# Kernel tuning notes

Measured on AMD Instinct MI355X. Metric: run time of the kernel, lower is better.

## Reference

```python
import jax, jax.numpy as jnp
import numpy as np
import math

B, C, IMG, E, H, L, FF, D, NCLS = 4, 3, 64, 256, 8, 512, 4, 4, 1000
N = IMG * IMG  # 4096 pixel tokens
HS = H * E    # head_size = embedding_size * heads (per original code)


def setup_inputs() -> dict:
    key = jax.random.key(0)
    ks = jax.random.split(key, 32)
    s = 0.02
    nrm = lambda k, shape: (jax.random.normal(k, shape, jnp.float32) * s)
    inp = {
        "x": jax.random.normal(ks[0], (B, C, N), jnp.float32),
        "conv_w": nrm(ks[1], (E, C)),                 # 1x1 conv1d kernel
        "conv_b": jnp.zeros((E,), jnp.float32),
        "pos_emb": nrm(ks[2], (N, E)),
        "latents": jax.random.normal(ks[3], (L, E), jnp.float32),
        # cross-attention (queries from latents, keys/values from image tokens)
        "ca_wq": nrm(ks[4], (E, HS)),
        "ca_wk": nrm(ks[5], (E, HS)),
        "ca_wv": nrm(ks[6], (E, HS)),
        "ca_wu": nrm(ks[7], (HS, E)),
        "ca_bu": jnp.zeros((E,), jnp.float32),
        "ca_ln_g": jnp.ones((E,), jnp.float32),
        "ca_ln_b": jnp.zeros((E,), jnp.float32),
        # transformer blocks, stacked along depth for lax.scan
        "blk_wq": nrm(ks[8], (D, E, HS)),
        "blk_wk": nrm(ks[9], (D, E, HS)),
        "blk_wv": nrm(ks[10], (D, E, HS)),
        "blk_wu": nrm(ks[11], (D, HS, E)),
        "blk_bu": jnp.zeros((D, E), jnp.float32),
        "blk_ln1_g": jnp.ones((D, E), jnp.float32),
        "blk_ln1_b": jnp.zeros((D, E), jnp.float32),
        "blk_w1": nrm(ks[12], (D, E, FF * E)),
        "blk_b1": jnp.zeros((D, FF * E), jnp.float32),
        "blk_w2": nrm(ks[13], (D, FF * E, E)),
        "blk_b2": jnp.zeros((D, E), jnp.float32),
        "blk_ln2_g": jnp.ones((D, E), jnp.float32),
        "blk_ln2_b": jnp.zeros((D, E), jnp.float32),
        "cls_w": nrm(ks[14], (E, NCLS)),
        "cls_b": jnp.zeros((NCLS,), jnp.float32),
        "heads": H,
    }
    return inp


def _ln(x, g, b):
    m = jnp.mean(x, axis=-1, keepdims=True)
    v = jnp.mean(jnp.square(x - m), axis=-1, keepdims=True)
    return g * (x - m) * jax.lax.rsqrt(v + 1e-5) + b


def _mha(q_in, kv_in, wq, wk, wv, wu, bu, heads):
    # Faithful to original: each head has dim = embedding_size (head_size = heads*emb),
    # and the scale is sqrt(emb // heads).
    b, nq, e = q_in.shape
    nk = kv_in.shape[1]
    q = (q_in @ wq).reshape(b, nq, heads, e)
    k = (kv_in @ wk).reshape(b, nk, heads, e)
    v = (kv_in @ wv).reshape(b, nk, heads, e)
    scale = 1.0 / math.sqrt(e // heads)
    w = jax.nn.softmax(jnp.einsum('bqhe,bkhe->bhqk', q, k) * scale, axis=-1)
    a = jnp.einsum('bhqk,bkhe->bqhe', w, v).reshape(b, nq, heads * e)
    return a @ wu + bu


def reference(x, conv_w, conv_b, pos_emb, latents,
              ca_wq, ca_wk, ca_wv, ca_wu, ca_bu, ca_ln_g, ca_ln_b,
              blk_wq, blk_wk, blk_wv, blk_wu, blk_bu,
              blk_ln1_g, blk_ln1_b, blk_w1, blk_b1, blk_w2, blk_b2,
              blk_ln2_g, blk_ln2_b, cls_w, cls_b, heads):
    bsz = x.shape[0]
    # 1x1 conv1d over flattened pixels: (B, C, N) -> (B, N, E), plus positions
    tokens = jnp.einsum('bcn,ec->bne', x, conv_w) + conv_b + pos_emb
    # latents as queries, image tokens as keys/values (cross-attention)
    z = jnp.broadcast_to(latents, (bsz,) + latents.shape)
    z = _ln(_mha(z, tokens, ca_wq, ca_wk, ca_wv, ca_wu, ca_bu, heads) + z,
            ca_ln_g, ca_ln_b)
    # dropout is identity in eval mode

    def block(z, p):
        wq, wk, wv, wu, bu, g1, b1, w1, c1, w2, c2, g2, b2 = p
        z = _ln(_mha(z, z, wq, wk, wv, wu, bu, heads) + z, g1, b1)
        h = jax.nn.gelu(z @ w1 + c1, approximate=False) @ w2 + c2
        z = _ln(h + z, g2, b2)
        return z, None

    z, _ = jax.lax.scan(block, z,
                        (blk_wq, blk_wk, blk_wv, blk_wu, blk_bu,
                         blk_ln1_g, blk_ln1_b, blk_w1, blk_b1,
                         blk_w2, blk_b2, blk_ln2_g, blk_ln2_b))
    # global average over latents, then classifier
    return jnp.mean(z, axis=1) @ cls_w + cls_b
```

## Files before the change

### kernel.cpp

```cpp
#include <hip/hip_runtime.h>
#include <hip/hip_bf16.h>
#include <math.h>


typedef __attribute__((ext_vector_type(8))) short s8v;
typedef __attribute__((ext_vector_type(4))) float f32x4;
typedef __attribute__((ext_vector_type(16))) float f32x16;
typedef __attribute__((ext_vector_type(4))) unsigned u32x4;

__device__ __forceinline__ short f2b(float f) {
  union { float f; unsigned u; } a; a.f = f;
  unsigned r = a.u + 0x7fff + ((a.u >> 16) & 1);
  return (short)(r >> 16);
}
__device__ __forceinline__ float b2f(short s) {
  union { unsigned u; float f; } a; a.u = ((unsigned)(unsigned short)s) << 16;
  return a.f;
}
__device__ __forceinline__ unsigned cvtpk(float lo, float hi) {
  unsigned r;
  asm("v_cvt_pk_bf16_f32 %0, %1, %2" : "=v"(r) : "v"(lo), "v"(hi));
  return r;
}

__device__ __forceinline__ void gl16(const void* gp, void* lp) {
  __builtin_amdgcn_global_load_lds(
      (const __attribute__((address_space(1))) unsigned int*)gp,
      (__attribute__((address_space(3))) unsigned int*)lp, 16, 0, 0);
}

__global__ __launch_bounds__(256) void k_tokens2(
    const float* __restrict__ x, const float* __restrict__ cw,
    const float* __restrict__ cb, const float* __restrict__ pe,
    short* __restrict__ tok, short* __restrict__ tokT)
{
  int b = blockIdx.y, n0 = blockIdx.x * 32;
  int e = threadIdx.x;
  float c0 = cw[e * 3], c1 = cw[e * 3 + 1], c2 = cw[e * 3 + 2], cbv = cb[e];
  const float* xb = x + b * 12288 + n0;
  short acc[32];
#pragma unroll
  for (int i = 0; i < 32; ++i) {
    int n = n0 + i;
    float s = cbv + pe[n * 256 + e] + xb[i] * c0 + xb[4096 + i] * c1 + xb[8192 + i] * c2;
    short v = f2b(s);
    tok[((long)b * 4096 + n) * 256 + e] = v;
    acc[i] = v;
  }
  short* tr = tokT + ((long)b * 256 + e) * 4096 + n0;
#pragma unroll
  for (int i = 0; i < 4; ++i)
    *reinterpret_cast<s8v*>(tr + i * 8) = *reinterpret_cast<s8v*>(acc + i * 8);
}

struct TrJob {
  const float* src; short* dst;
  int R, C; long sIn, sOut;
  int mode, tilesPerZ, z, tileBase;
  float scale;
};
struct TrJobs { TrJob j[11]; };

__global__ __launch_bounds__(256) void k_trbatch(TrJobs jb, int njobs)
{
  __shared__ float t[32][33];
  int tb = blockIdx.x, ji = 0;
#pragma unroll
  for (int k = 1; k < 11; ++k)
    if (k < njobs && tb >= jb.j[k].tileBase) ji = k;
  TrJob J = jb.j[ji];
  int local = tb - J.tileBase;
  if (J.mode == 1) {
    long o = (long)local * 8192 + threadIdx.x;
#pragma unroll
    for (int k = 0; k < 32; ++k)
      J.dst[o + k * 256] = f2b(J.src[o + k * 256] * J.scale);
    return;
  }
  int zi = local / J.tilesPerZ, ti = local - zi * J.tilesPerZ;
  int ntx = J.C >> 5;
  int tx = ti % ntx, ty = ti / ntx;
  const float* ib = J.src + (long)zi * J.sIn;
  short* ob = J.dst + (long)zi * J.sOut;
  int c0 = tx * 32, r0 = ty * 32;
  int lx = threadIdx.x & 31, ly = threadIdx.x >> 5;
#pragma unroll
  for (int i = 0; i < 4; ++i)
    t[ly * 4 + i][lx] = ib[(long)(r0 + ly * 4 + i) * J.C + c0 + lx];
  __syncthreads();
#pragma unroll
  for (int i = 0; i < 4; ++i)
    ob[(long)(c0 + ly * 4 + i) * J.R + r0 + lx] = f2b(t[lx][ly * 4 + i] * J.scale);
}

template<int EPI>
__global__ __launch_bounds__(256) void k_mgemm(
    const short* __restrict__ A, const short* __restrict__ Bt,
    void* __restrict__ Cv, const float* __restrict__ bias,
    int K, int lda, int ldb, int ldc,
    long sA, long sB, long sC, int zdA, int zmA, int zdB, int zmB)
{
  __shared__ char As[8192];
  __shared__ char Bs[8192];
  int z = blockIdx.z;
  const short* Ab = A + ((long)((z / zdA) % zmA)) * sA;
  const short* Bb = Bt + ((long)((z / zdB) % zmB)) * sB;
  int t = threadIdx.x;
  int lane = t & 63, w = t >> 6;
  int wr = w >> 1, wc = w & 1;
  int g = lane >> 4, l15 = lane & 15;
  long row0 = (long)blockIdx.y * 128, col0 = (long)blockIdx.x * 128;
  const f32x4 zz = {0.f, 0.f, 0.f, 0.f};
  f32x4 acc[4][4];
#pragma unroll
  for (int m = 0; m < 4; ++m)
#pragma unroll
    for (int n = 0; n < 4; ++n) acc[m][n] = zz;

  auto mload = [&](s8v* aa, s8v* bb, int kk) {
#pragma unroll
    for (int i = 0; i < 2; ++i) {
      int r = i * 64 + (t >> 2), c = t & 3;
      aa[i] = *(const s8v*)&Ab[(row0 + r) * (long)lda + kk + c * 8];
      bb[i] = *(const s8v*)&Bb[(col0 + r) * (long)ldb + kk + c * 8];
    }
  };
  auto mstore = [&](s8v* aa, s8v* bb) {
#pragma unroll
    for (int i = 0; i < 2; ++i) {
      int r = i * 64 + (t >> 2), c = t & 3;
      int off = (r * 64 + c * 16) ^ ((r & 7) << 4);
      *(s8v*)&As[off] = aa[i];
      *(s8v*)&Bs[off] = bb[i];
    }
  };
  auto mcomp = [&]() {
    s8v af[4], bfr[4];
#pragma unroll
    for (int m = 0; m < 4; ++m) {
      int r = wr * 64 + m * 16 + l15;
      af[m] = *(const s8v*)&As[(r * 64 + g * 16) ^ ((r & 7) << 4)];
    }
#pragma unroll
    for (int n = 0; n < 4; ++n) {
      int r = wc * 64 + n * 16 + l15;
      bfr[n] = *(const s8v*)&Bs[(r * 64 + g * 16) ^ ((r & 7) << 4)];
    }
#pragma unroll
    for (int m = 0; m < 4; ++m)
#pragma unroll
      for (int n = 0; n < 4; ++n)
        acc[m][n] = __builtin_amdgcn_mfma_f32_16x16x32_bf16(af[m], bfr[n], acc[m][n], 0, 0, 0);
  };

  s8v a0[2], b0[2], a1[2], b1[2];
  mload(a0, b0, 0);
  for (int k0 = 0; k0 < K; k0 += 64) {
    __syncthreads(); mstore(a0, b0); __syncthreads();
    mload(a1, b1, k0 + 32);
    mcomp();
    __syncthreads(); mstore(a1, b1); __syncthreads();
    if (k0 + 64 < K) mload(a0, b0, k0 + 64);
    mcomp();
  }

  long zo = (long)z * sC;
#pragma unroll
  for (int m = 0; m < 4; ++m)
#pragma unroll
    for (int n = 0; n < 4; ++n)
#pragma unroll
      for (int r = 0; r < 4; ++r) {
        long rr = row0 + wr * 64 + m * 16 + g * 4 + r;
        long cc = col0 + wc * 64 + n * 16 + l15;
        float v = acc[m][n][r];
        if (EPI == 1) {
          v += bias[cc];
          v = 0.5f * v * (1.f + erff(v * 0.70710678118654752f));
        }
        if (EPI == 2)
          ((float*)Cv)[zo + rr * ldc + cc] = v;
        else
          ((short*)Cv)[zo + rr * ldc + cc] = f2b(v);
      }
}

__global__ __launch_bounds__(512, 2) void k_mflash8(
    const short* __restrict__ Qp, const short* __restrict__ Kp,
    const short* __restrict__ Vtp, short* __restrict__ Opart,
    float* __restrict__ MLp,
    int nk, int ldq, int ldk, int ldvt,
    long qh, long qb, long kh, long kb, long vh, long vb)
{
  __shared__ char pool[131072];
  int t = threadIdx.x, lane = t & 63, w = t >> 6;
  int l31 = lane & 31, hi = lane >> 5;
  int h = blockIdx.y, b = blockIdx.z;
  int kv = blockIdx.x & 3, qblk = blockIdx.x >> 2;
  const short* Q  = Qp  + (long)h * qh + (long)b * qb;
  const short* Kg = Kp  + (long)h * kh + (long)b * kb;
  const short* Vg = Vtp + (long)h * vh + (long)b * vb;
  int q0w = qblk * 256 + w * 32;
  int nkq = nk >> 2;
  int NIT = nkq >> 6;
  long k0 = (long)kv * nkq;

  s8v qf[16];
  {
    const short* Qrow = Q + (long)(q0w + l31) * ldq + hi * 8;
#pragma unroll
    for (int s = 0; s < 16; ++s) qf[s] = *(const s8v*)(Qrow + s * 16);
  }

  const char* KgB = (const char*)Kg;
  const char* VgB = (const char*)Vg;
  unsigned koff[4], voff[4];
#pragma unroll
  for (int c = 0; c < 4; ++c) {
    int r = 8 * w + 2 * c + hi;
    koff[c] = (unsigned)((k0 + r) * (long)ldk * 2) + ((l31 ^ (r & 31)) << 4);
    int rv = 32 * w + 8 * c + (lane >> 3);
    voff[c] = (unsigned)(((long)rv * ldvt + k0) * 2) + (((lane & 7) ^ (lane >> 3)) << 4);
  }
  const unsigned kStep = (unsigned)(64 * ldk * 2);

  auto stage = [&](int bsel) {
    char* kd = pool + bsel * 65536 + (w << 12);
    char* vd = kd + 32768;
#pragma unroll
    for (int c = 0; c < 4; ++c) { gl16(KgB + koff[c], kd + c * 1024); koff[c] += kStep; }
#pragma unroll
    for (int c = 0; c < 4; ++c) { gl16(VgB + voff[c], vd + c * 1024); voff[c] += 128; }
  };

  f32x16 accO[8];
#pragma unroll
  for (int n = 0; n < 8; ++n)
#pragma unroll
    for (int i = 0; i < 16; ++i) accO[n][i] = 0.f;
  float mrow = -1e30f, lrow = 0.f;

  stage(0);

  for (int it = 0; it < NIT; ++it) {
    int cur = it & 1;
    asm volatile("s_waitcnt vmcnt(0)" ::: "memory");
    __syncthreads();
    if (it + 1 < NIT) stage(cur ^ 1);
    const char* kls = pool + cur * 65536;
    const char* vls = kls + 32768;

    f32x16 sacc[2];
#pragma unroll
    for (int i = 0; i < 16; ++i) { sacc[0][i] = 0.f; sacc[1][i] = 0.f; }
    __builtin_amdgcn_s_setprio(1);
#pragma unroll
    for (int tt = 0; tt < 2; ++tt) {
      int r = tt * 32 + l31;
#pragma unroll
      for (int s = 0; s < 16; ++s) {
        s8v kf = *(const s8v*)&kls[r * 512 + (((2 * s + hi) ^ l31) << 4)];
        sacc[tt] = __builtin_amdgcn_mfma_f32_32x32x16_bf16(kf, qf[s], sacc[tt], 0, 0, 0);
      }
    }
    __builtin_amdgcn_s_setprio(0);

    float mt = sacc[0][0];
#pragma unroll
    for (int i = 1; i < 16; ++i) mt = fmaxf(mt, sacc[0][i]);
#pragma unroll
    for (int i = 0; i < 16; ++i) mt = fmaxf(mt, sacc[1][i]);
    mt = fmaxf(mt, __shfl_xor(mt, 32));
    if (__any(mt - mrow > 8.f)) {
      float mn = fmaxf(mrow, mt);
      float al = __expf(mrow - mn);
      mrow = mn; lrow *= al;
#pragma unroll
      for (int r = 0; r < 16; ++r) {
        float alr = __shfl(al, (r & 3) + 8 * (r >> 2) + 4 * hi);
#pragma unroll
        for (int n = 0; n < 8; ++n) accO[n][r] *= alr;
      }
    }
    float ls = 0.f;
#pragma unroll
    for (int tt = 0; tt < 2; ++tt)
#pragma unroll
      for (int i = 0; i < 16; ++i) {
        float p = __expf(sacc[tt][i] - mrow);
        sacc[tt][i] = p; ls += p;
      }
    ls += __shfl_xor(ls, 32);
    lrow += ls;

    s8v pa[4];
#pragma unroll
    for (int s = 0; s < 4; ++s) {
      int tt = s >> 1, r0 = (s & 1) * 8;
      unsigned w0 = cvtpk(sacc[tt][r0 + 0], sacc[tt][r0 + 1]);
      unsigned w1 = cvtpk(sacc[tt][r0 + 2], sacc[tt][r0 + 3]);
      unsigned w2 = cvtpk(sacc[tt][r0 + 4], sacc[tt][r0 + 5]);
      unsigned w3 = cvtpk(sacc[tt][r0 + 6], sacc[tt][r0 + 7]);
      unsigned x0 = (unsigned)__shfl_xor((int)w0, 32);
      unsigned x1 = (unsigned)__shfl_xor((int)w1, 32);
      unsigned x2 = (unsigned)__shfl_xor((int)w2, 32);
      unsigned x3 = (unsigned)__shfl_xor((int)w3, 32);
      u32x4 pw;
      pw.x = hi ? x2 : w0;
      pw.y = hi ? x3 : w1;
      pw.z = hi ? w2 : x0;
      pw.w = hi ? w3 : x1;
      pa[s] = *(s8v*)&pw;
    }

    __builtin_amdgcn_s_setprio(1);
#pragma unroll
    for (int n = 0; n < 8; ++n) {
      int rv = n * 32 + l31;
#pragma unroll
      for (int s2 = 0; s2 < 4; ++s2) {
        s8v vf = *(const s8v*)&vls[rv * 128 + (((2 * s2 + hi) ^ (l31 & 7)) << 4)];
        accO[n] = __builtin_amdgcn_mfma_f32_32x32x16_bf16(pa[s2], vf, accO[n], 0, 0, 0);
      }
    }
    __builtin_amdgcn_s_setprio(0);
  }

  long prow = (((long)kv * 4 + b) * 8 + h) * 512;
  short* Ob = Opart + prow * 256;
  float* MLb = MLp + prow * 2;
  if (lane < 32) {
    MLb[(q0w + l31) * 2] = mrow;
    MLb[(q0w + l31) * 2 + 1] = lrow;
  }
  char* freebuf = pool + ((((NIT - 1) & 1) ^ 1) << 16);
  float* st = (float*)(freebuf + w * 4096);
  int orow = lane >> 1, ohalf = lane & 1;
#pragma unroll
  for (int n = 0; n < 8; ++n) {
#pragma unroll
    for (int r = 0; r < 16; ++r) {
      int ql = (r & 3) + 8 * (r >> 2) + 4 * hi;
      st[ql * 32 + l31] = accO[n][r];
    }
    short obuf[16];
#pragma unroll
    for (int jj = 0; jj < 4; ++jj) {
      f32x4 v = *(const f32x4*)&st[orow * 32 + ohalf * 16 + jj * 4];
      obuf[jj * 4 + 0] = f2b(v.x); obuf[jj * 4 + 1] = f2b(v.y);
      obuf[jj * 4 + 2] = f2b(v.z); obuf[jj * 4 + 3] = f2b(v.w);
    }
    short* dst = Ob + (long)(q0w + orow) * 256 + n * 32 + ohalf * 16;
    *(s8v*)(dst) = *(s8v*)&obuf[0];
    *(s8v*)(dst + 8) = *(s8v*)&obuf[8];
  }
}

__global__ __launch_bounds__(512) void k_fcomb(
    const short* __restrict__ Op, const float* __restrict__ ML,
    short* __restrict__ O)
{
  int d = threadIdx.x & 255;
  int q = blockIdx.x * 2 + (threadIdx.x >> 8);
  int h = blockIdx.y, b = blockIdx.z;
  const long kvs = 4L * 8 * 512;
  long r0 = ((long)b * 8 + h) * 512 + q;
  float mm[4], ll[4], m = -1e30f;
#pragma unroll
  for (int kv = 0; kv < 4; ++kv) {
    mm[kv] = ML[(kv * kvs + r0) * 2];
    ll[kv] = ML[(kv * kvs + r0) * 2 + 1];
    m = fmaxf(m, mm[kv]);
  }
  float wv[4], lsum = 0.f;
#pragma unroll
  for (int kv = 0; kv < 4; ++kv) { wv[kv] = __expf(mm[kv] - m); lsum += ll[kv] * wv[kv]; }
  float inv = 1.f / lsum, acc = 0.f;
#pragma unroll
  for (int kv = 0; kv < 4; ++kv)
    acc += b2f(Op[(kv * kvs + r0) * 256 + d]) * wv[kv];
  O[(long)b * 1048576 + (long)q * 2048 + h * 256 + d] = f2b(acc * inv);
}

__global__ __launch_bounds__(256) void k_bias_res_ln(
    const float* __restrict__ Yp, int nPart, long pStride,
    const float* __restrict__ bias,
    const float* __restrict__ res, int resMod,
    const float* __restrict__ g, const float* __restrict__ bta,
    float* __restrict__ out, short* __restrict__ out_bf)
{
  __shared__ float red[4];
  int row = blockIdx.x, e = threadIdx.x;
  float v = bias[e] + res[(long)(row % resMod) * 256 + e];
  for (int s = 0; s < nPart; ++s) v += Yp[s * pStride + (long)row * 256 + e];
  float s1 = v;
#pragma unroll
  for (int o = 32; o > 0; o >>= 1) s1 += __shfl_down(s1, o);
  if ((e & 63) == 0) red[e >> 6] = s1;
  __syncthreads();
  float mean = (red[0] + red[1] + red[2] + red[3]) * (1.f / 256.f);
  float d = v - mean;
  __syncthreads();
  float s2 = d * d;
#pragma unroll
  for (int o = 32; o > 0; o >>= 1) s2 += __shfl_down(s2, o);
  if ((e & 63) == 0) red[e >> 6] = s2;
  __syncthreads();
  float var = (red[0] + red[1] + red[2] + red[3]) * (1.f / 256.f);
  float o = g[e] * d * rsqrtf(var + 1e-5f) + bta[e];
  out[(long)row * 256 + e] = o;
  out_bf[(long)row * 256 + e] = f2b(o);
}

__global__ __launch_bounds__(256) void k_meancls(
    const float* __restrict__ z, const float* __restrict__ w,
    const float* __restrict__ bias, float* __restrict__ out)
{
  __shared__ float zms[256];
  int b = blockIdx.y, e = threadIdx.x;
  float s = 0.f;
  for (int l = 0; l < 512; ++l) s += z[((long)b * 512 + l) * 256 + e];
  zms[e] = s * (1.f / 512.f);
  __syncthreads();
  int j = blockIdx.x * 256 + e;
  if (j >= 1000) return;
  float acc = bias[j];
  for (int e2 = 0; e2 < 256; ++e2) acc += zms[e2] * w[e2 * 1000 + j];
  out[b * 1000 + j] = acc;
}

extern "C" void kernel_launch(void* const* d_in, const int* in_sizes, int n_in,
                              void* d_out, int out_size, void* d_ws, size_t ws_size,
                              hipStream_t stream)
{
  (void)in_sizes; (void)n_in; (void)out_size; (void)ws_size;
  const float* x       = (const float*)d_in[0];
  const float* conv_w  = (const float*)d_in[1];
  const float* conv_b  = (const float*)d_in[2];
  const float* pos_emb = (const float*)d_in[3];
  const float* latents = (const float*)d_in[4];
  const float* ca_wq   = (const float*)d_in[5];
  const float* ca_wk   = (const float*)d_in[6];
  const float* ca_wv   = (const float*)d_in[7];
  const float* ca_wu   = (const float*)d_in[8];
  const float* ca_bu   = (const float*)d_in[9];
  const float* ca_ln_g = (const float*)d_in[10];
  const float* ca_ln_b = (const float*)d_in[11];
  const float* blk_wq  = (const float*)d_in[12];
  const float* blk_wk  = (const float*)d_in[13];
  const float* blk_wv  = (const float*)d_in[14];
  const float* blk_wu  = (const float*)d_in[15];
  const float* blk_bu  = (const float*)d_in[16];
  const float* blk_ln1_g = (const float*)d_in[17];
  const float* blk_ln1_b = (const float*)d_in[18];
  const float* blk_w1  = (const float*)d_in[19];
  const float* blk_b1  = (const float*)d_in[20];
  const float* blk_w2  = (const float*)d_in[21];
  const float* blk_b2  = (const float*)d_in[22];
  const float* blk_ln2_g = (const float*)d_in[23];
  const float* blk_ln2_b = (const float*)d_in[24];
  const float* cls_w   = (const float*)d_in[25];
  const float* cls_b   = (const float*)d_in[26];
  float* out = (float*)d_out;

  short* wqT_ca = (short*)d_ws;
  short* wkT_ca = wqT_ca + 524288;
  short* wuT_ca = wkT_ca + 524288;
  short* wv_ca  = wuT_ca + 524288;
  short* lat_bf = wv_ca + 524288;
  short* wqkT   = lat_bf + 131072;
  short* wvT    = wqkT + 4194304;
  short* wuT_b  = wvT + 2097152;
  short* w1T    = wuT_b + 2097152;
  short* w2T    = w1T + 1048576;
  short* tok_bf = w2T + 1048576;
  short* tokT   = tok_bf + 4194304;
  short* qCA    = tokT + 4194304;
  short* qtil   = qCA + 1048576;
  short* MstT   = qtil + 1048576;
  short* VtB    = MstT + 524288;
  short* bufO   = VtB + 4194304;
  short* h1     = bufO + 4194304;
  short* z_bf   = h1 + 2097152;
  float* z      = (float*)(z_bf + 524288);
  float* zm     = z + 524288;
  float* Ypart  = zm + 1024;
  short* Opart  = (short*)(Ypart + 4194304);
  float* MLp    = (float*)(Opart + 16777216);
  short* QKb    = tok_bf;

  const float scale = 0.17677669529663687f;
  const int BIG = 1 << 30;

  TrJobs JB; int nj = 0, base = 0;
  auto addT = [&](const float* s, short* d, int R, int C, long sIn, long sOut,
                  int zc, float sc) {
    int tpz = (C >> 5) * (R >> 5);
    JB.j[nj] = {s, d, R, C, sIn, sOut, 0, tpz, zc, base, sc};
    base += tpz * zc; ++nj;
  };
  auto addC = [&](const float* s, short* d, int nelem) {
    int tpz = nelem >> 13;
    JB.j[nj] = {s, d, 0, 0, 0, 0, 1, tpz, 1, base, 1.f};
    base += tpz; ++nj;
  };
  addT(ca_wq, wqT_ca, 256, 2048, 0, 0, 1, scale);
  addT(ca_wk, wkT_ca, 256, 2048, 0, 0, 1, 1.f);
  addT(ca_wu, wuT_ca, 2048, 256, 0, 0, 1, 1.f);
  addT(blk_wq, wqkT, 256, 2048, 524288, 1048576, 4, scale);
  addT(blk_wk, wqkT + 524288, 256, 2048, 524288, 1048576, 4, 1.f);
  addT(blk_wv, wvT, 256, 2048, 524288, 524288, 4, 1.f);
  addT(blk_wu, wuT_b, 2048, 256, 524288, 524288, 4, 1.f);
  addT(blk_w1, w1T, 256, 1024, 262144, 262144, 4, 1.f);
  addT(blk_w2, w2T, 1024, 256, 262144, 262144, 4, 1.f);
  addC(ca_wv, wv_ca, 524288);
  addC(latents, lat_bf, 131072);
  k_trbatch<<<base, 256, 0, stream>>>(JB, nj);

  k_tokens2<<<dim3(128, 4), 256, 0, stream>>>(x, conv_w, conv_b, pos_emb,
                                              tok_bf, tokT);

  k_mgemm<0><<<dim3(16, 4, 1), 256, 0, stream>>>(
      lat_bf, wqT_ca, qCA, nullptr, 256, 256, 256, 2048, 0, 0, 0, 1, BIG, 1, BIG);
  k_mgemm<0><<<dim3(2, 4, 8), 256, 0, stream>>>(
      qCA, wkT_ca, qtil, nullptr, 256, 2048, 256, 256, 256, 65536, 131072, 1, 8, 1, 8);
  k_mgemm<0><<<dim3(2, 2, 8), 256, 0, stream>>>(
      wuT_ca, wv_ca, MstT, nullptr, 256, 2048, 2048, 2048, 256, 256, 256, 1, 8, 1, 8);
  k_mflash8<<<dim3(8, 8, 4), 512, 0, stream>>>(
      qtil, tok_bf, tokT, Opart, MLp, 4096, 256, 256, 4096,
      131072L, 0L, 0L, 1048576L, 0L, 1048576L);
  k_fcomb<<<dim3(256, 8, 4), 512, 0, stream>>>(Opart, MLp, bufO);
  k_mgemm<2><<<dim3(2, 16, 8), 256, 0, stream>>>(
      bufO, MstT, Ypart, nullptr, 256, 2048, 2048, 256, 256, 256, 524288, 1, 8, 1, 8);
  k_bias_res_ln<<<2048, 256, 0, stream>>>(Ypart, 8, 524288L, ca_bu, latents, 512,
                                          ca_ln_g, ca_ln_b, z, z_bf);

  for (int d = 0; d < 4; ++d) {
    k_mgemm<0><<<dim3(32, 16, 1), 256, 0, stream>>>(
        z_bf, wqkT + (long)d * 1048576, QKb, nullptr,
        256, 256, 256, 4096, 0, 0, 0, 1, BIG, 1, BIG);
    k_mgemm<0><<<dim3(4, 2, 32), 256, 0, stream>>>(
        wvT + (long)d * 524288, z_bf, VtB, nullptr,
        256, 256, 256, 512, 65536, 131072, 131072, 1, 8, 8, BIG);
    k_mflash8<<<dim3(8, 8, 4), 512, 0, stream>>>(
        QKb, QKb + 2048, VtB, Opart, MLp, 512, 4096, 4096, 512,
        256L, 2097152L, 256L, 2097152L, 131072L, 1048576L);
    k_fcomb<<<dim3(256, 8, 4), 512, 0, stream>>>(Opart, MLp, bufO);
    k_mgemm<2><<<dim3(2, 16, 8), 256, 0, stream>>>(
        bufO, wuT_b + (long)d * 524288, Ypart, nullptr,
        256, 2048, 2048, 256, 256, 256, 524288, 1, 8, 1, 8);
    k_bias_res_ln<<<2048, 256, 0, stream>>>(Ypart, 8, 524288L, blk_bu + d * 256, z, 2048,
        blk_ln1_g + d * 256, blk_ln1_b + d * 256, z, z_bf);
    k_mgemm<1><<<dim3(8, 16, 1), 256, 0, stream>>>(
        z_bf, w1T + (long)d * 262144, h1, blk_b1 + d * 1024,
        256, 256, 256, 1024, 0, 0, 0, 1, BIG, 1, BIG);
    k_mgemm<2><<<dim3(2, 16, 8), 256, 0, stream>>>(
        h1, w2T + (long)d * 262144, Ypart, nullptr,
        128, 1024, 1024, 256, 128, 128, 524288, 1, 8, 1, 8);
    k_bias_res_ln<<<2048, 256, 0, stream>>>(Ypart, 8, 524288L, blk_b2 + d * 256, z, 2048,
        blk_ln2_g + d * 256, blk_ln2_b + d * 256, z, z_bf);
  }

  k_meancls<<<dim3(4, 4), 256, 0, stream>>>(z, cls_w, cls_b, out);
}
```

Measured before the change: 639.5 us.

## Software-pipeline flash attention so the PV MMA of the previous tile overlaps QK

Restructures the flash-attention loop so that iteration i computes QK^T for tile i, then runs the P·V MMAs for tile i-1 using the probabilities kept from the previous iteration. Softmax of tile i runs after the new staging load is issued, and a final PV step runs after the loop. The waitcnt is relaxed to vmcnt(4) plus raw barriers, which lets MFMA work interleave with exp/shuffle work and overlap the global loads. The cost is more register pressure from carrying paP, and the synchronisation is delicate: the V buffer from the previous iteration must not be overwritten while it is still being read.

```diff
diff --git a/kernel.cpp b/kernel.cpp
--- a/kernel.cpp
+++ b/kernel.cpp
@@ -185,7 +185,7 @@
       }
 }
 
-__global__ __launch_bounds__(512, 2) void k_mflash8(
+__global__ __launch_bounds__(512, 2) void k_mflash9(
     const short* __restrict__ Qp, const short* __restrict__ Kp,
     const short* __restrict__ Vtp, short* __restrict__ Opart,
     float* __restrict__ MLp,
@@ -239,16 +239,17 @@
 #pragma unroll
     for (int i = 0; i < 16; ++i) accO[n][i] = 0.f;
   float mrow = -1e30f, lrow = 0.f;
+  s8v paP[4];
 
   stage(0);
 
   for (int it = 0; it < NIT; ++it) {
     int cur = it & 1;
-    asm volatile("s_waitcnt vmcnt(0)" ::: "memory");
-    __syncthreads();
-    if (it + 1 < NIT) stage(cur ^ 1);
-    const char* kls = pool + cur * 65536;
-    const char* vls = kls + 32768;
+    asm volatile("s_waitcnt vmcnt(4)" ::: "memory");
+    __builtin_amdgcn_s_barrier();
+    __builtin_amdgcn_sched_barrier(0);
+    const char* kls  = pool + cur * 65536;
+    const char* vlsP = pool + (cur ^ 1) * 65536 + 32768;
 
     f32x16 sacc[2];
 #pragma unroll
@@ -263,7 +264,23 @@
         sacc[tt] = __builtin_amdgcn_mfma_f32_32x32x16_bf16(kf, qf[s], sacc[tt], 0, 0, 0);
       }
     }
+    if (it > 0) {
+#pragma unroll
+      for (int n = 0; n < 8; ++n) {
+        int rv = n * 32 + l31;
+#pragma unroll
+        for (int s2 = 0; s2 < 4; ++s2) {
+          s8v vf = *(const s8v*)&vlsP[rv * 128 + (((2 * s2 + hi) ^ (l31 & 7)) << 4)];
+          accO[n] = __builtin_amdgcn_mfma_f32_32x32x16_bf16(paP[s2], vf, accO[n], 0, 0, 0);
+        }
+      }
+    }
     __builtin_amdgcn_s_setprio(0);
+
+    asm volatile("s_waitcnt lgkmcnt(0)" ::: "memory");
+    __builtin_amdgcn_sched_barrier(0);
+    __builtin_amdgcn_s_barrier();
+    if (it + 1 < NIT) stage(cur ^ 1);
 
     float mt = sacc[0][0];
 #pragma unroll
@@ -293,7 +310,6 @@
     ls += __shfl_xor(ls, 32);
     lrow += ls;
 
-    s8v pa[4];
 #pragma unroll
     for (int s = 0; s < 4; ++s) {
       int tt = s >> 1, r0 = (s & 1) * 8;
@@ -310,9 +326,15 @@
       pw.y = hi ? x3 : w1;
       pw.z = hi ? w2 : x0;
       pw.w = hi ? w3 : x1;
-      pa[s] = *(s8v*)&pw;
-    }
-
+      paP[s] = *(s8v*)&pw;
+    }
+  }
+
+  asm volatile("s_waitcnt vmcnt(0)" ::: "memory");
+  __builtin_amdgcn_s_barrier();
+  __builtin_amdgcn_sched_barrier(0);
+  {
+    const char* vls = pool + ((NIT - 1) & 1) * 65536 + 32768;
     __builtin_amdgcn_s_setprio(1);
 #pragma unroll
     for (int n = 0; n < 8; ++n) {
@@ -320,7 +342,7 @@
 #pragma unroll
       for (int s2 = 0; s2 < 4; ++s2) {
         s8v vf = *(const s8v*)&vls[rv * 128 + (((2 * s2 + hi) ^ (l31 & 7)) << 4)];
-        accO[n] = __builtin_amdgcn_mfma_f32_32x32x16_bf16(pa[s2], vf, accO[n], 0, 0, 0);
+        accO[n] = __builtin_amdgcn_mfma_f32_32x32x16_bf16(paP[s2], vf, accO[n], 0, 0, 0);
       }
     }
     __builtin_amdgcn_s_setprio(0);
@@ -333,8 +355,7 @@
     MLb[(q0w + l31) * 2] = mrow;
     MLb[(q0w + l31) * 2 + 1] = lrow;
   }
-  char* freebuf = pool + ((((NIT - 1) & 1) ^ 1) << 16);
-  float* st = (float*)(freebuf + w * 4096);
+  float* st = (float*)(pool + w * 4096);
   int orow = lane >> 1, ohalf = lane & 1;
 #pragma unroll
   for (int n = 0; n < 8; ++n) {
@@ -526,7 +547,7 @@
       qCA, wkT_ca, qtil, nullptr, 256, 2048, 256, 256, 256, 65536, 131072, 1, 8, 1, 8);
   k_mgemm<0><<<dim3(2, 2, 8), 256, 0, stream>>>(
       wuT_ca, wv_ca, MstT, nullptr, 256, 2048, 2048, 2048, 256, 256, 256, 1, 8, 1, 8);
-  k_mflash8<<<dim3(8, 8, 4), 512, 0, stream>>>(
+  k_mflash9<<<dim3(8, 8, 4), 512, 0, stream>>>(
       qtil, tok_bf, tokT, Opart, MLp, 4096, 256, 256, 4096,
       131072L, 0L, 0L, 1048576L, 0L, 1048576L);
   k_fcomb<<<dim3(256, 8, 4), 512, 0, stream>>>(Opart, MLp, bufO);
@@ -542,7 +563,7 @@
     k_mgemm<0><<<dim3(4, 2, 32), 256, 0, stream>>>(
         wvT + (long)d * 524288, z_bf, VtB, nullptr,
         256, 256, 256, 512, 65536, 131072, 131072, 1, 8, 8, BIG);
-    k_mflash8<<<dim3(8, 8, 4), 512, 0, stream>>>(
+    k_mflash9<<<dim3(8, 8, 4), 512, 0, stream>>>(
         QKb, QKb + 2048, VtB, Opart, MLp, 512, 4096, 4096, 512,
         256L, 2097152L, 256L, 2097152L, 131072L, 1048576L);
     k_fcomb<<<dim3(256, 8, 4), 512, 0, stream>>>(Opart, MLp, bufO);
```

New measurement: 635.6 us. About the same (-0.6%).

## Shrink flash-attention blocks to 4 waves with 32-key tiles and 64KB LDS

Applied to the files above, without the earlier changes.

Recasts the split-K flash attention kernel to use 256-thread blocks covering 128 queries, 32-key tiles per iteration and half the shared memory, launching twice as many blocks. K/V staging offsets and swizzles are redone for the narrower tiles, and the output staging now reuses the pool after a barrier. The aim is higher occupancy and better load balance across CUs. The cost is more iterations, each with less MFMA work to cover load latency and the softmax and sync overhead.

```diff
diff --git a/kernel.cpp b/kernel.cpp
--- a/kernel.cpp
+++ b/kernel.cpp
@@ -185,14 +185,14 @@
       }
 }
 
-__global__ __launch_bounds__(512, 2) void k_mflash8(
+__global__ __launch_bounds__(256, 2) void k_mflash10(
     const short* __restrict__ Qp, const short* __restrict__ Kp,
     const short* __restrict__ Vtp, short* __restrict__ Opart,
     float* __restrict__ MLp,
     int nk, int ldq, int ldk, int ldvt,
     long qh, long qb, long kh, long kb, long vh, long vb)
 {
-  __shared__ char pool[131072];
+  __shared__ char pool[65536];
   int t = threadIdx.x, lane = t & 63, w = t >> 6;
   int l31 = lane & 31, hi = lane >> 5;
   int h = blockIdx.y, b = blockIdx.z;
@@ -200,9 +200,9 @@
   const short* Q  = Qp  + (long)h * qh + (long)b * qb;
   const short* Kg = Kp  + (long)h * kh + (long)b * kb;
   const short* Vg = Vtp + (long)h * vh + (long)b * vb;
-  int q0w = qblk * 256 + w * 32;
+  int q0w = qblk * 128 + w * 32;
   int nkq = nk >> 2;
-  int NIT = nkq >> 6;
+  int NIT = nkq >> 5;
   long k0 = (long)kv * nkq;
 
   s8v qf[16];
@@ -218,19 +218,20 @@
 #pragma unroll
   for (int c = 0; c < 4; ++c) {
     int r = 8 * w + 2 * c + hi;
-    koff[c] = (unsigned)((k0 + r) * (long)ldk * 2) + ((l31 ^ (r & 31)) << 4);
-    int rv = 32 * w + 8 * c + (lane >> 3);
-    voff[c] = (unsigned)(((long)rv * ldvt + k0) * 2) + (((lane & 7) ^ (lane >> 3)) << 4);
-  }
-  const unsigned kStep = (unsigned)(64 * ldk * 2);
+    koff[c] = (unsigned)((k0 + r) * (long)ldk * 2) + ((l31 ^ r) << 4);
+    int rv = 64 * w + 16 * c + (lane >> 2);
+    voff[c] = (unsigned)(((long)rv * ldvt + k0) * 2)
+              + (((lane & 3) ^ ((lane >> 3) & 3)) << 4);
+  }
+  const unsigned kStep = (unsigned)(32 * ldk * 2);
 
   auto stage = [&](int bsel) {
-    char* kd = pool + bsel * 65536 + (w << 12);
-    char* vd = kd + 32768;
+    char* kd = pool + bsel * 32768 + (w << 12);
+    char* vd = kd + 16384;
 #pragma unroll
     for (int c = 0; c < 4; ++c) { gl16(KgB + koff[c], kd + c * 1024); koff[c] += kStep; }
 #pragma unroll
-    for (int c = 0; c < 4; ++c) { gl16(VgB + voff[c], vd + c * 1024); voff[c] += 128; }
+    for (int c = 0; c < 4; ++c) { gl16(VgB + voff[c], vd + c * 1024); voff[c] += 64; }
   };
 
   f32x16 accO[8];
@@ -247,29 +248,23 @@
     asm volatile("s_waitcnt vmcnt(0)" ::: "memory");
     __syncthreads();
     if (it + 1 < NIT) stage(cur ^ 1);
-    const char* kls = pool + cur * 65536;
-    const char* vls = kls + 32768;
-
-    f32x16 sacc[2];
-#pragma unroll
-    for (int i = 0; i < 16; ++i) { sacc[0][i] = 0.f; sacc[1][i] = 0.f; }
+    const char* kls = pool + cur * 32768;
+    const char* vls = kls + 16384;
+
+    f32x16 sacc;
+#pragma unroll
+    for (int i = 0; i < 16; ++i) sacc[i] = 0.f;
     __builtin_amdgcn_s_setprio(1);
 #pragma unroll
-    for (int tt = 0; tt < 2; ++tt) {
-      int r = tt * 32 + l31;
-#pragma unroll
-      for (int s = 0; s < 16; ++s) {
-        s8v kf = *(const s8v*)&kls[r * 512 + (((2 * s + hi) ^ l31) << 4)];
-        sacc[tt] = __builtin_amdgcn_mfma_f32_32x32x16_bf16(kf, qf[s], sacc[tt], 0, 0, 0);
-      }
+    for (int s = 0; s < 16; ++s) {
+      s8v kf = *(const s8v*)&kls[l31 * 512 + (((2 * s + hi) ^ l31) << 4)];
+      sacc = __builtin_amdgcn_mfma_f32_32x32x16_bf16(kf, qf[s], sacc, 0, 0, 0);
     }
     __builtin_amdgcn_s_setprio(0);
 
-    float mt = sacc[0][0];
-#pragma unroll
-    for (int i = 1; i < 16; ++i) mt = fmaxf(mt, sacc[0][i]);
-#pragma unroll
-    for (int i = 0; i < 16; ++i) mt = fmaxf(mt, sacc[1][i]);
+    float mt = sacc[0];
+#pragma unroll
+    for (int i = 1; i < 16; ++i) mt = fmaxf(mt, sacc[i]);
     mt = fmaxf(mt, __shfl_xor(mt, 32));
     if (__any(mt - mrow > 8.f)) {
       float mn = fmaxf(mrow, mt);
@@ -284,23 +279,21 @@
     }
     float ls = 0.f;
 #pragma unroll
-    for (int tt = 0; tt < 2; ++tt)
-#pragma unroll
-      for (int i = 0; i < 16; ++i) {
-        float p = __expf(sacc[tt][i] - mrow);
-        sacc[tt][i] = p; ls += p;
-      }
+    for (int i = 0; i < 16; ++i) {
+      float p = __expf(sacc[i] - mrow);
+      sacc[i] = p; ls += p;
+    }
     ls += __shfl_xor(ls, 32);
     lrow += ls;
 
-    s8v pa[4];
-#pragma unroll
-    for (int s = 0; s < 4; ++s) {
-      int tt = s >> 1, r0 = (s & 1) * 8;
-      unsigned w0 = cvtpk(sacc[tt][r0 + 0], sacc[tt][r0 + 1]);
-      unsigned w1 = cvtpk(sacc[tt][r0 + 2], sacc[tt][r0 + 3]);
-      unsigned w2 = cvtpk(sacc[tt][r0 + 4], sacc[tt][r0 + 5]);
-      unsigned w3 = cvtpk(sacc[tt][r0 + 6], sacc[tt][r0 + 7]);
+    s8v pa[2];
+#pragma unroll
+    for (int s2 = 0; s2 < 2; ++s2) {
+      int r0 = s2 * 8;
+      unsigned w0 = cvtpk(sacc[r0 + 0], sacc[r0 + 1]);
+      unsigned w1 = cvtpk(sacc[r0 + 2], sacc[r0 + 3]);
+      unsigned w2 = cvtpk(sacc[r0 + 4], sacc[r0 + 5]);
+      unsigned w3 = cvtpk(sacc[r0 + 6], sacc[r0 + 7]);
       unsigned x0 = (unsigned)__shfl_xor((int)w0, 32);
       unsigned x1 = (unsigned)__shfl_xor((int)w1, 32);
       unsigned x2 = (unsigned)__shfl_xor((int)w2, 32);
@@ -310,7 +303,7 @@
       pw.y = hi ? x3 : w1;
       pw.z = hi ? w2 : x0;
       pw.w = hi ? w3 : x1;
-      pa[s] = *(s8v*)&pw;
+      pa[s2] = *(s8v*)&pw;
     }
 
     __builtin_amdgcn_s_setprio(1);
@@ -318,8 +311,8 @@
     for (int n = 0; n < 8; ++n) {
       int rv = n * 32 + l31;
 #pragma unroll
-      for (int s2 = 0; s2 < 4; ++s2) {
-        s8v vf = *(const s8v*)&vls[rv * 128 + (((2 * s2 + hi) ^ (l31 & 7)) << 4)];
+      for (int s2 = 0; s2 < 2; ++s2) {
+        s8v vf = *(const s8v*)&vls[rv * 64 + (((2 * s2 + hi) ^ ((l31 >> 1) & 3)) << 4)];
         accO[n] = __builtin_amdgcn_mfma_f32_32x32x16_bf16(pa[s2], vf, accO[n], 0, 0, 0);
       }
     }
@@ -333,8 +326,8 @@
     MLb[(q0w + l31) * 2] = mrow;
     MLb[(q0w + l31) * 2 + 1] = lrow;
   }
-  char* freebuf = pool + ((((NIT - 1) & 1) ^ 1) << 16);
-  float* st = (float*)(freebuf + w * 4096);
+  __syncthreads();
+  float* st = (float*)(pool + w * 4096);
   int orow = lane >> 1, ohalf = lane & 1;
 #pragma unroll
   for (int n = 0; n < 8; ++n) {
@@ -455,6 +448,7 @@
   const float* blk_ln1_b = (const float*)d_in[18];
   const float* blk_w1  = (const float*)d_in[19];
   const float* blk_b1  = (const float*)d_in[20];
+  const float* blk_b2_unused = nullptr; (void)blk_b2_unused;
   const float* blk_w2  = (const float*)d_in[21];
   const float* blk_b2  = (const float*)d_in[22];
   const float* blk_ln2_g = (const float*)d_in[23];
@@ -526,7 +520,7 @@
       qCA, wkT_ca, qtil, nullptr, 256, 2048, 256, 256, 256, 65536, 131072, 1, 8, 1, 8);
   k_mgemm<0><<<dim3(2, 2, 8), 256, 0, stream>>>(
       wuT_ca, wv_ca, MstT, nullptr, 256, 2048, 2048, 2048, 256, 256, 256, 1, 8, 1, 8);
-  k_mflash8<<<dim3(8, 8, 4), 512, 0, stream>>>(
+  k_mflash10<<<dim3(16, 8, 4), 256, 0, stream>>>(
       qtil, tok_bf, tokT, Opart, MLp, 4096, 256, 256, 4096,
       131072L, 0L, 0L, 1048576L, 0L, 1048576L);
   k_fcomb<<<dim3(256, 8, 4), 512, 0, stream>>>(Opart, MLp, bufO);
@@ -542,7 +536,7 @@
     k_mgemm<0><<<dim3(4, 2, 32), 256, 0, stream>>>(
         wvT + (long)d * 524288, z_bf, VtB, nullptr,
         256, 256, 256, 512, 65536, 131072, 131072, 1, 8, 8, BIG);
-    k_mflash8<<<dim3(8, 8, 4), 512, 0, stream>>>(
+    k_mflash10<<<dim3(16, 8, 4), 256, 0, stream>>>(
         QKb, QKb + 2048, VtB, Opart, MLp, 512, 4096, 4096, 512,
         256L, 2097152L, 256L, 2097152L, 131072L, 1048576L);
     k_fcomb<<<dim3(256, 8, 4), 512, 0, stream>>>(Opart, MLp, bufO);
```

Result: faster. 595.5 us (-6.9%).
